# Performance work log

Hardware: AMD Instinct MI355X
Metric: run time of the kernel (lower is better)

## Reference

```python
import jax, jax.numpy as jnp
import numpy as np
import math

EMBED_DIM = 1024
NUM_HEADS = 16
HEAD_DIM = EMBED_DIM // NUM_HEADS
BLOCK_SIZE = 64
N_GLOBAL = 8


def _sparse_mask(seq_len: int) -> jnp.ndarray:
    """Block-diagonal local mask + 8 global tokens (rows and cols), bool [S, S]."""
    idx = jnp.arange(seq_len)
    block_id = idx // BLOCK_SIZE
    local = block_id[:, None] == block_id[None, :]
    # torch.linspace(0, S-1, min(8, S)).long() -> truncated evenly spaced positions
    gp = np.linspace(0, seq_len - 1, min(N_GLOBAL, seq_len)).astype(np.int64)
    is_global = jnp.zeros((seq_len,), dtype=bool).at[jnp.asarray(gp)].set(True)
    return local | is_global[:, None] | is_global[None, :]


def setup_inputs() -> dict:
    key = jax.random.key(0)
    ks = jax.random.split(key, 9)
    E = EMBED_DIM
    s = 0.02
    return {
        "x": jax.random.normal(ks[0], (1, 4096, E), dtype=jnp.float32),
        "Wq": jax.random.normal(ks[1], (E, E), dtype=jnp.float32) * s,
        "bq": jnp.zeros((E,), dtype=jnp.float32),
        "Wk": jax.random.normal(ks[2], (E, E), dtype=jnp.float32) * s,
        "bk": jnp.zeros((E,), dtype=jnp.float32),
        "Wv": jax.random.normal(ks[3], (E, E), dtype=jnp.float32) * s,
        "bv": jnp.zeros((E,), dtype=jnp.float32),
        "Wo": jax.random.normal(ks[4], (E, E), dtype=jnp.float32) * s,
        "bo": jnp.zeros((E,), dtype=jnp.float32),
    }


def reference(x, Wq, bq, Wk, bk, Wv, bv, Wo, bo):
    B, S, E = x.shape
    H, D = NUM_HEADS, HEAD_DIM
    mask = _sparse_mask(S)  # [S, S] bool

    def split_heads(y):
        return y.reshape(B, S, H, D).transpose(0, 2, 1, 3)  # [B,H,S,D]

    q = split_heads(x @ Wq + bq)
    k = split_heads(x @ Wk + bk)
    v = split_heads(x @ Wv + bv)

    scale = math.sqrt(D)
    scores = jnp.einsum("bhqd,bhkd->bhqk", q, k) / scale  # [B,H,S,S]
    scores = jnp.where(mask[None, None], scores, -jnp.inf)
    attn = jax.nn.softmax(scores, axis=-1)  # every row has its diagonal block -> no NaN
    out = jnp.einsum("bhqk,bhkd->bhqd", attn, v)
    out = out.transpose(0, 2, 1, 3).reshape(B, S, E)
    return out @ Wo + bo
```

## Files before the change

kernel.cpp:

```cpp
#include <hip/hip_runtime.h>

typedef __attribute__((ext_vector_type(8))) short short8;
typedef __attribute__((ext_vector_type(8))) __bf16 bf16x8;
typedef __attribute__((ext_vector_type(4))) float f32x4;

#define S_LEN 4096
#define EMB   1024
#define NHEAD 16
#define HDIM  64
#define GCHUNK 256
#define NCHUNK (S_LEN / GCHUNK)

__constant__ int GPOS[8] = {0, 585, 1170, 1755, 2340, 2925, 3510, 4095};

__device__ __forceinline__ unsigned short f2bf(float f) {
    unsigned int u = __float_as_uint(f);
    u += 0x7fffu + ((u >> 16) & 1u);
    return (unsigned short)(u >> 16);
}
__device__ __forceinline__ float bf2f(unsigned short s) {
    return __uint_as_float(((unsigned int)s) << 16);
}
#define GLOAD16(src, dst) __builtin_amdgcn_global_load_lds( \
    (const __attribute__((address_space(1))) void*)(src),    \
    (__attribute__((address_space(3))) void*)(dst), 16, 0, 0)

__global__ __launch_bounds__(256) void convert_x_kernel(const float4* __restrict__ in,
                                                        ushort4* __restrict__ out, int n4) {
    for (int i = blockIdx.x * blockDim.x + threadIdx.x; i < n4; i += gridDim.x * blockDim.x) {
        float4 v = in[i];
        ushort4 o;
        o.x = f2bf(v.x); o.y = f2bf(v.y); o.z = f2bf(v.z); o.w = f2bf(v.w);
        out[i] = o;
    }
}

__global__ __launch_bounds__(256) void convert_w_kernel(const float* __restrict__ W0,
                                                        const float* __restrict__ W1,
                                                        const float* __restrict__ W2,
                                                        const float* __restrict__ W3,
                                                        unsigned short* __restrict__ wt) {
    __shared__ float tile[64][65];
    const int bx = blockIdx.x;
    const int w = bx >> 8, rem = bx & 255;
    const int k0 = (rem >> 4) * 64, n0 = (rem & 15) * 64;
    const float* W = (w == 0) ? W0 : (w == 1) ? W1 : (w == 2) ? W2 : W3;
    unsigned short* dst = wt + (size_t)w * (1u << 20);
    const int t = threadIdx.x;
    for (int i = t; i < 4096; i += 256) {
        int r = i >> 6, c = i & 63;
        tile[r][c] = W[(size_t)(k0 + r) * EMB + n0 + c];
    }
    __syncthreads();
    for (int i = t; i < 4096; i += 256) {
        int r = i >> 6, c = i & 63;
        dst[(size_t)(n0 + r) * EMB + k0 + c] = f2bf(tile[c][r]);
    }
}

__global__ __launch_bounds__(256) void vtrans(const unsigned short* __restrict__ vb,
                                              unsigned short* __restrict__ vtg) {
    __shared__ unsigned short tile[64][72];
    const int t = threadIdx.x;
    const int h = blockIdx.x >> 6;
    const int s0 = (blockIdx.x & 63) * 64;
    for (int i = t; i < 512; i += 256) {
        int r = i >> 3, c = i & 7;
        *(short8*)&tile[r][c * 8] = *(const short8*)(vb + (size_t)(s0 + r) * EMB + h * 64 + c * 8);
    }
    __syncthreads();
    for (int i = t; i < 512; i += 256) {
        int d = i >> 3, c = i & 7;
        short8 v;
#pragma unroll
        for (int j = 0; j < 8; ++j) v[j] = (short)tile[c * 8 + j][d];
        *(short8*)(vtg + (size_t)(h * 64 + d) * S_LEN + s0 + c * 8) = v;
    }
}

__global__ __launch_bounds__(256) void gemm_qkv(const unsigned short* __restrict__ A,
                                                const unsigned short* __restrict__ Bt,
                                                const float* __restrict__ bq,
                                                const float* __restrict__ bk,
                                                const float* __restrict__ bv,
                                                unsigned short* __restrict__ qb,
                                                unsigned short* __restrict__ kb,
                                                unsigned short* __restrict__ vb) {
    __shared__ unsigned short As[128 * 64];
    __shared__ unsigned short Bs[128 * 64];
    const int t = threadIdx.x;
    const int lane = t & 63;
    const int wave = t >> 6;
    const int wm = wave >> 1, wn = wave & 1;
    const int col16 = lane & 15, grp = lane >> 4;
    const int bm = blockIdx.x / 24;
    const int bn = blockIdx.x % 24;
    const int sel = bn >> 3, bn_l = bn & 7;
    const float* bias = (sel == 0) ? bq : (sel == 1) ? bk : bv;
    unsigned short* out = (sel == 0) ? qb : (sel == 1) ? kb : vb;

    f32x4 acc[4][4] = {};

    for (int k0 = 0; k0 < EMB; k0 += 64) {
        __syncthreads();
#pragma unroll
        for (int c = 0; c < 8; ++c) {
            int p = t + 256 * (c & 3);
            int row = p >> 3, s = p & 7, kc = s ^ (row & 7);
            if (c < 4) {
                GLOAD16(A + (size_t)(bm * 128 + row) * EMB + k0 + kc * 8, As + p * 8);
            } else {
                GLOAD16(Bt + (size_t)(bn * 128 + row) * EMB + k0 + kc * 8, Bs + p * 8);
            }
        }
        asm volatile("s_waitcnt vmcnt(0)" ::: "memory");
        __syncthreads();
#pragma unroll
        for (int kk = 0; kk < 2; ++kk) {
            const int kc = kk * 4 + grp;
            bf16x8 af[4], bfr[4];
#pragma unroll
            for (int f = 0; f < 4; ++f) {
                int mrow = wm * 64 + f * 16 + col16;
                short8 ra = *(const short8*)(As + (mrow * 8 + (kc ^ (mrow & 7))) * 8);
                af[f] = __builtin_bit_cast(bf16x8, ra);
                int nrow = wn * 64 + f * 16 + col16;
                short8 rb = *(const short8*)(Bs + (nrow * 8 + (kc ^ (nrow & 7))) * 8);
                bfr[f] = __builtin_bit_cast(bf16x8, rb);
            }
#pragma unroll
            for (int fi = 0; fi < 4; ++fi)
#pragma unroll
                for (int fj = 0; fj < 4; ++fj)
                    acc[fi][fj] = __builtin_amdgcn_mfma_f32_16x16x32_bf16(af[fi], bfr[fj], acc[fi][fj], 0, 0, 0);
        }
    }

#pragma unroll
    for (int fi = 0; fi < 4; ++fi) {
        const int row0 = bm * 128 + wm * 64 + fi * 16 + grp * 4;
#pragma unroll
        for (int fj = 0; fj < 4; ++fj) {
            const int col = bn_l * 128 + wn * 64 + fj * 16 + col16;
            const float bvv = bias[col];
#pragma unroll
            for (int r = 0; r < 4; ++r)
                out[(size_t)(row0 + r) * EMB + col] = f2bf(acc[fi][fj][r] + bvv);
        }
    }
}

__global__ __launch_bounds__(256) void gemm_bt_f32(const unsigned short* __restrict__ A,
                                                   const unsigned short* __restrict__ Bt,
                                                   const float* __restrict__ bias,
                                                   float* __restrict__ Cout) {
    __shared__ unsigned short As[128 * 64];
    __shared__ unsigned short Bs[64 * 64];
    const int t = threadIdx.x;
    const int lane = t & 63;
    const int wave = t >> 6;
    const int wm = wave >> 1, wn = wave & 1;
    const int bm = blockIdx.x >> 4;
    const int bn = blockIdx.x & 15;

    f32x4 acc[4][2] = {};

    for (int k0 = 0; k0 < EMB; k0 += 64) {
        __syncthreads();
#pragma unroll
        for (int c = 0; c < 6; ++c) {
            const unsigned short* src;
            unsigned short* dst;
            if (c < 4) {
                int p = t + 256 * c;
                int m = p >> 3, s = p & 7;
                int kc = s ^ (m & 7);
                src = A + (size_t)(bm * 128 + m) * EMB + k0 + kc * 8;
                dst = As + p * 8;
            } else {
                int p = t + 256 * (c - 4);
                int n = p >> 3, s = p & 7;
                int kc = s ^ (n & 7);
                src = Bt + (size_t)(bn * 64 + n) * EMB + k0 + kc * 8;
                dst = Bs + p * 8;
            }
            GLOAD16(src, dst);
        }
        asm volatile("s_waitcnt vmcnt(0)" ::: "memory");
        __syncthreads();
#pragma unroll
        for (int kk = 0; kk < 2; ++kk) {
            const int kc = kk * 4 + (lane >> 4);
            bf16x8 af[4], bfr[2];
#pragma unroll
            for (int f = 0; f < 4; ++f) {
                int mrow = wm * 64 + f * 16 + (lane & 15);
                short8 ra = *(const short8*)(As + mrow * 64 + ((kc ^ (mrow & 7)) * 8));
                af[f] = __builtin_bit_cast(bf16x8, ra);
            }
#pragma unroll
            for (int f = 0; f < 2; ++f) {
                int nrow = wn * 32 + f * 16 + (lane & 15);
                short8 rb = *(const short8*)(Bs + nrow * 64 + ((kc ^ (nrow & 7)) * 8));
                bfr[f] = __builtin_bit_cast(bf16x8, rb);
            }
#pragma unroll
            for (int fi = 0; fi < 4; ++fi)
#pragma unroll
                for (int fj = 0; fj < 2; ++fj)
                    acc[fi][fj] = __builtin_amdgcn_mfma_f32_16x16x32_bf16(af[fi], bfr[fj], acc[fi][fj], 0, 0, 0);
        }
    }

#pragma unroll
    for (int fi = 0; fi < 4; ++fi) {
        const int row0 = bm * 128 + wm * 64 + fi * 16 + (lane >> 4) * 4;
#pragma unroll
        for (int fj = 0; fj < 2; ++fj) {
            const int col = bn * 64 + wn * 32 + fj * 16 + (lane & 15);
            const float bvv = bias[col];
#pragma unroll
            for (int r = 0; r < 4; ++r)
                Cout[(size_t)(row0 + r) * EMB + col] = acc[fi][fj][r] + bvv;
        }
    }
}

__global__ __launch_bounds__(256) void attn_local(const unsigned short* __restrict__ qb,
                                                  const unsigned short* __restrict__ kb,
                                                  const unsigned short* __restrict__ vb,
                                                  const unsigned short* __restrict__ vtg,
                                                  unsigned short* __restrict__ ab) {
    __shared__ unsigned short Qs[64 * 64];
    __shared__ unsigned short Ks[80 * 64];
    __shared__ unsigned short Vts[64 * 64];
    __shared__ unsigned short Ps[64 * 64];
    __shared__ float Pg[64][9];
    __shared__ float Vg[8][64];

    const int t = threadIdx.x;
    const int lane = t & 63, wave = t >> 6;
    const int col16 = lane & 15, grp = lane >> 4;
    const int h = blockIdx.x >> 6, b = blockIdx.x & 63;
    const int bc = h * 64;

#pragma unroll
    for (int c = 0; c < 2; ++c) {
        int p = t + 256 * c, row = p >> 3, s = p & 7, kc = s ^ (row & 7);
        GLOAD16(qb + (size_t)(b * 64 + row) * EMB + bc + kc * 8, Qs + p * 8);
    }
#pragma unroll
    for (int c = 0; c < 3; ++c) {
        int p = t + 256 * c;
        if (p < 576) {
            int row = p >> 3, s = p & 7, kc = s ^ (row & 7);
            int srow = (row < 64) ? (b * 64 + row) : GPOS[row - 64];
            GLOAD16(kb + (size_t)srow * EMB + bc + kc * 8, Ks + p * 8);
        }
    }
    if (t < 64) {
        short8 z = {};
        *(short8*)(Ks + (576 + t) * 8) = z;
    }
#pragma unroll
    for (int c = 0; c < 2; ++c) {
        int p = t + 256 * c, row = p >> 3, s = p & 7, kc = s ^ (row & 7);
        GLOAD16(vtg + (size_t)(bc + row) * S_LEN + b * 64 + kc * 8, Vts + p * 8);
    }
    for (int i = t; i < 512; i += 256) {
        int g = i >> 6, d = i & 63;
        Vg[g][d] = bf2f(vb[(size_t)GPOS[g] * EMB + bc + d]);
    }
    asm volatile("s_waitcnt vmcnt(0)" ::: "memory");
    __syncthreads();

    f32x4 sc[5] = {};
    const int arow = wave * 16 + col16;
#pragma unroll
    for (int kk = 0; kk < 2; ++kk) {
        const int kc = kk * 4 + (lane >> 4);
        short8 ra = *(const short8*)(Qs + (arow * 8 + (kc ^ (arow & 7))) * 8);
        bf16x8 af = __builtin_bit_cast(bf16x8, ra);
#pragma unroll
        for (int n = 0; n < 5; ++n) {
            const int brow = n * 16 + col16;
            short8 rb = *(const short8*)(Ks + (brow * 8 + (kc ^ (brow & 7))) * 8);
            sc[n] = __builtin_amdgcn_mfma_f32_16x16x32_bf16(af, __builtin_bit_cast(bf16x8, rb), sc[n], 0, 0, 0);
        }
    }

    const bool valid4 = (col16 < 8) && ((GPOS[col16] >> 6) != b);
#pragma unroll
    for (int r = 0; r < 4; ++r) {
        const int row = wave * 16 + grp * 4 + r;
        float s[5];
#pragma unroll
        for (int n = 0; n < 4; ++n) s[n] = sc[n][r] * 0.125f;
        s[4] = valid4 ? sc[4][r] * 0.125f : -1e30f;
        float m = fmaxf(fmaxf(fmaxf(s[0], s[1]), fmaxf(s[2], s[3])), s[4]);
#pragma unroll
        for (int off = 1; off < 16; off <<= 1) m = fmaxf(m, __shfl_xor(m, off));
        float e[5], l = 0.f;
#pragma unroll
        for (int n = 0; n < 5; ++n) { e[n] = __expf(s[n] - m); l += e[n]; }
#pragma unroll
        for (int off = 1; off < 16; off <<= 1) l += __shfl_xor(l, off);
        const float inv = 1.f / l;
#pragma unroll
        for (int n = 0; n < 4; ++n) {
            const int col = n * 16 + col16;
            const int kc = col >> 3;
            Ps[(row * 8 + (kc ^ (row & 7))) * 8 + (col & 7)] = f2bf(e[n] * inv);
        }
        if (col16 < 8) Pg[row][col16] = e[4] * inv;
    }
    __syncthreads();

    f32x4 oa[4] = {};
#pragma unroll
    for (int kk = 0; kk < 2; ++kk) {
        const int kc = kk * 4 + (lane >> 4);
        short8 ra = *(const short8*)(Ps + (arow * 8 + (kc ^ (arow & 7))) * 8);
        bf16x8 af = __builtin_bit_cast(bf16x8, ra);
#pragma unroll
        for (int n = 0; n < 4; ++n) {
            const int drow = n * 16 + col16;
            short8 rb = *(const short8*)(Vts + (drow * 8 + (kc ^ (drow & 7))) * 8);
            oa[n] = __builtin_amdgcn_mfma_f32_16x16x32_bf16(af, __builtin_bit_cast(bf16x8, rb), oa[n], 0, 0, 0);
        }
    }

    float pgr[4][8];
#pragma unroll
    for (int r = 0; r < 4; ++r) {
        const int row = wave * 16 + grp * 4 + r;
#pragma unroll
        for (int g = 0; g < 8; ++g) pgr[r][g] = Pg[row][g];
    }
#pragma unroll
    for (int n = 0; n < 4; ++n) {
        const int d = n * 16 + col16;
#pragma unroll
        for (int g = 0; g < 8; ++g) {
            const float vg = Vg[g][d];
#pragma unroll
            for (int r = 0; r < 4; ++r) oa[n][r] += pgr[r][g] * vg;
        }
    }

#pragma unroll
    for (int n = 0; n < 4; ++n) {
        const int d = n * 16 + col16;
#pragma unroll
        for (int r = 0; r < 4; ++r) {
            const int row = wave * 16 + grp * 4 + r;
            ab[(size_t)(b * 64 + row) * EMB + bc + d] = f2bf(oa[n][r]);
        }
    }
}

__global__ __launch_bounds__(256) void attn_gpart(const unsigned short* __restrict__ qb,
                                                  const unsigned short* __restrict__ kb,
                                                  const unsigned short* __restrict__ vb,
                                                  float* __restrict__ o_part,
                                                  float* __restrict__ m_l) {
    __shared__ float Qs[8][64];
    __shared__ unsigned short Vs[GCHUNK][64];
    __shared__ float Ps[8][GCHUNK];
    __shared__ float mfin[8], lfin[8];
    const int t = threadIdx.x;
    const int lane = t & 63;
    const int wave = t >> 6;
    const int h = blockIdx.x >> 4;
    const int ch = blockIdx.x & (NCHUNK - 1);
    const int bc = h * 64;
    const int k0 = ch * GCHUNK;

    for (int i = t; i < 512; i += 256) {
        int r = i >> 6, d = i & 63;
        Qs[r][d] = bf2f(qb[(size_t)GPOS[r] * EMB + bc + d]);
    }
    {
        const unsigned short* vrow = vb + (size_t)(k0 + t) * EMB + bc;
#pragma unroll
        for (int c = 0; c < 8; ++c) {
            short8 vv = *(const short8*)(vrow + c * 8);
            *(short8*)(&Vs[t][(c ^ (t & 7)) * 8]) = vv;
        }
    }
    float kf[64];
    {
        const unsigned short* krow = kb + (size_t)(k0 + t) * EMB + bc;
#pragma unroll
        for (int c = 0; c < 8; ++c) {
            short8 kv = *(const short8*)(krow + c * 8);
#pragma unroll
            for (int j = 0; j < 8; ++j) kf[c * 8 + j] = bf2f((unsigned short)kv[j]);
        }
    }
    __syncthreads();

#pragma unroll
    for (int r = 0; r < 8; ++r) {
        float a0 = 0.f, a1 = 0.f, a2 = 0.f, a3 = 0.f;
#pragma unroll
        for (int c4 = 0; c4 < 16; ++c4) {
            f32x4 q = *(const f32x4*)&Qs[r][c4 * 4];
            a0 += q.x * kf[c4 * 4 + 0];
            a1 += q.y * kf[c4 * 4 + 1];
            a2 += q.z * kf[c4 * 4 + 2];
            a3 += q.w * kf[c4 * 4 + 3];
        }
        Ps[r][t] = (a0 + a1 + a2 + a3) * 0.125f;
    }
    __syncthreads();

#pragma unroll
    for (int rr = 0; rr < 2; ++rr) {
        const int r = wave * 2 + rr;
        float v0 = Ps[r][lane], v1 = Ps[r][lane + 64], v2 = Ps[r][lane + 128], v3 = Ps[r][lane + 192];
        float m = fmaxf(fmaxf(v0, v1), fmaxf(v2, v3));
#pragma unroll
        for (int off = 1; off < 64; off <<= 1) m = fmaxf(m, __shfl_xor(m, off));
        float e0 = __expf(v0 - m), e1 = __expf(v1 - m), e2 = __expf(v2 - m), e3 = __expf(v3 - m);
        float l = e0 + e1 + e2 + e3;
#pragma unroll
        for (int off = 1; off < 64; off <<= 1) l += __shfl_xor(l, off);
        Ps[r][lane] = e0; Ps[r][lane + 64] = e1; Ps[r][lane + 128] = e2; Ps[r][lane + 192] = e3;
        if (lane == 0) { mfin[r] = m; lfin[r] = l; }
    }
    __syncthreads();

    const int r = t >> 5;
    const int d0 = (t & 31) * 2;
    const int cc = d0 >> 3, ee = d0 & 7;
    float acc0 = 0.f, acc1 = 0.f;
    for (int k = 0; k < GCHUNK; k += 4) {
        f32x4 p = *(const f32x4*)&Ps[r][k];
#pragma unroll
        for (int j = 0; j < 4; ++j) {
            unsigned int vv = *(const unsigned int*)&Vs[k + j][((cc ^ ((k + j) & 7)) << 3) + ee];
            acc0 += p[j] * bf2f((unsigned short)(vv & 0xffff));
            acc1 += p[j] * bf2f((unsigned short)(vv >> 16));
        }
    }
    const int rowg = h * 8 + r;
    float* od = o_part + ((size_t)rowg * NCHUNK + ch) * 64 + d0;
    od[0] = acc0; od[1] = acc1;
    if ((t & 31) == 0) {
        m_l[((size_t)rowg * NCHUNK + ch) * 2 + 0] = mfin[r];
        m_l[((size_t)rowg * NCHUNK + ch) * 2 + 1] = lfin[r];
    }
}

__global__ __launch_bounds__(256) void attn_gcomb(const float* __restrict__ o_part,
                                                  const float* __restrict__ m_l,
                                                  unsigned short* __restrict__ ab) {
    const int gid = blockIdx.x * 256 + threadIdx.x;
    const int row = gid >> 6, d = gid & 63;
    float M = -1e30f;
#pragma unroll
    for (int c = 0; c < NCHUNK; ++c) M = fmaxf(M, m_l[((size_t)row * NCHUNK + c) * 2]);
    float L = 0.f, o = 0.f;
#pragma unroll
    for (int c = 0; c < NCHUNK; ++c) {
        float w = __expf(m_l[((size_t)row * NCHUNK + c) * 2] - M);
        L += m_l[((size_t)row * NCHUNK + c) * 2 + 1] * w;
        o += o_part[((size_t)row * NCHUNK + c) * 64 + d] * w;
    }
    const int h = row >> 3, gi = row & 7;
    ab[(size_t)GPOS[gi] * EMB + h * 64 + d] = f2bf(o / L);
}

extern "C" void kernel_launch(void* const* d_in, const int* in_sizes, int n_in,
                              void* d_out, int out_size, void* d_ws, size_t ws_size,
                              hipStream_t stream) {
    const float* x  = (const float*)d_in[0];
    const float* Wq = (const float*)d_in[1];
    const float* bq = (const float*)d_in[2];
    const float* Wk = (const float*)d_in[3];
    const float* bk = (const float*)d_in[4];
    const float* Wv = (const float*)d_in[5];
    const float* bv = (const float*)d_in[6];
    const float* Wo = (const float*)d_in[7];
    const float* bo = (const float*)d_in[8];

    char* ws = (char*)d_ws;
    unsigned short* xb = (unsigned short*)ws;
    unsigned short* wt = (unsigned short*)(ws + (8u << 20));
    unsigned short* qb = (unsigned short*)(ws + (16u << 20));
    unsigned short* kb = (unsigned short*)(ws + (24u << 20));
    unsigned short* vb = (unsigned short*)(ws + (32u << 20));
    unsigned short* ab = xb;

    float* o_part = (float*)d_out;
    float* m_l    = (float*)d_out + 128 * NCHUNK * 64;
    unsigned short* vtg = (unsigned short*)((char*)d_out + (4u << 20));

    const int n4 = S_LEN * EMB / 4;
    convert_x_kernel<<<2048, 256, 0, stream>>>((const float4*)x, (ushort4*)xb, n4);
    convert_w_kernel<<<1024, 256, 0, stream>>>(Wq, Wk, Wv, Wo, wt);

    gemm_qkv<<<(S_LEN / 128) * 24, 256, 0, stream>>>(xb, wt, bq, bk, bv, qb, kb, vb);

    vtrans<<<1024, 256, 0, stream>>>(vb, vtg);
    attn_local<<<NHEAD * 64, 256, 0, stream>>>(qb, kb, vb, vtg, ab);
    attn_gpart<<<NHEAD * NCHUNK, 256, 0, stream>>>(qb, kb, vb, o_part, m_l);
    attn_gcomb<<<(128 * 64) / 256, 256, 0, stream>>>(o_part, m_l, ab);

    gemm_bt_f32<<<(S_LEN / 128) * 16, 256, 0, stream>>>(ab, wt + (3u << 20), bo, (float*)d_out);
}
```

Baseline: 109.5 us.

## Double-buffer LDS in QKV and output GEMMs and widen output tile

Both GEMM kernels now use two LDS buffers. The next K-slice is issued with global_load_lds while MFMAs run on the current slice, with a single barrier per iteration in place of the explicit vmcnt wait. The output projection GEMM also moves from 128x64 to 128x128 tiles, halving the grid to 256 blocks to improve operand reuse. The trade-offs are 64KB of LDS per block, which limits occupancy, and fewer blocks for the output GEMM. Correctness also relies on the barrier draining the outstanding LDS-DMA loads.

New measurement: 115.1 us. +5.2%, slower.

```diff
diff --git a/kernel.cpp b/kernel.cpp
--- a/kernel.cpp
+++ b/kernel.cpp
@@ -86,8 +86,8 @@
                                                 unsigned short* __restrict__ qb,
                                                 unsigned short* __restrict__ kb,
                                                 unsigned short* __restrict__ vb) {
-    __shared__ unsigned short As[128 * 64];
-    __shared__ unsigned short Bs[128 * 64];
+    __shared__ unsigned short As[2][128 * 64];
+    __shared__ unsigned short Bs[2][128 * 64];
     const int t = threadIdx.x;
     const int lane = t & 63;
     const int wave = t >> 6;
@@ -101,20 +101,31 @@
 
     f32x4 acc[4][4] = {};
 
-    for (int k0 = 0; k0 < EMB; k0 += 64) {
-        __syncthreads();
-#pragma unroll
-        for (int c = 0; c < 8; ++c) {
-            int p = t + 256 * (c & 3);
+    auto stage = [&](int buf, int tstep) {
+        const int k0 = tstep * 64;
+#pragma unroll
+        for (int c = 0; c < 4; ++c) {
+            int p = t + 256 * c;
             int row = p >> 3, s = p & 7, kc = s ^ (row & 7);
-            if (c < 4) {
-                GLOAD16(A + (size_t)(bm * 128 + row) * EMB + k0 + kc * 8, As + p * 8);
-            } else {
-                GLOAD16(Bt + (size_t)(bn * 128 + row) * EMB + k0 + kc * 8, Bs + p * 8);
-            }
-        }
-        asm volatile("s_waitcnt vmcnt(0)" ::: "memory");
-        __syncthreads();
+            GLOAD16(A + (size_t)(bm * 128 + row) * EMB + k0 + kc * 8, &As[buf][p * 8]);
+        }
+#pragma unroll
+        for (int c = 0; c < 4; ++c) {
+            int p = t + 256 * c;
+            int row = p >> 3, s = p & 7, kc = s ^ (row & 7);
+            GLOAD16(Bt + (size_t)(bn * 128 + row) * EMB + k0 + kc * 8, &Bs[buf][p * 8]);
+        }
+    };
+
+    stage(0, 0);
+    __syncthreads();
+
+#pragma unroll 2
+    for (int tstep = 0; tstep < 16; ++tstep) {
+        const int cur = tstep & 1;
+        if (tstep < 15) stage(cur ^ 1, tstep + 1);
+        const unsigned short* Ab = As[cur];
+        const unsigned short* Bb = Bs[cur];
 #pragma unroll
         for (int kk = 0; kk < 2; ++kk) {
             const int kc = kk * 4 + grp;
@@ -122,10 +133,10 @@
 #pragma unroll
             for (int f = 0; f < 4; ++f) {
                 int mrow = wm * 64 + f * 16 + col16;
-                short8 ra = *(const short8*)(As + (mrow * 8 + (kc ^ (mrow & 7))) * 8);
+                short8 ra = *(const short8*)(Ab + (mrow * 8 + (kc ^ (mrow & 7))) * 8);
                 af[f] = __builtin_bit_cast(bf16x8, ra);
                 int nrow = wn * 64 + f * 16 + col16;
-                short8 rb = *(const short8*)(Bs + (nrow * 8 + (kc ^ (nrow & 7))) * 8);
+                short8 rb = *(const short8*)(Bb + (nrow * 8 + (kc ^ (nrow & 7))) * 8);
                 bfr[f] = __builtin_bit_cast(bf16x8, rb);
             }
 #pragma unroll
@@ -134,6 +145,7 @@
                 for (int fj = 0; fj < 4; ++fj)
                     acc[fi][fj] = __builtin_amdgcn_mfma_f32_16x16x32_bf16(af[fi], bfr[fj], acc[fi][fj], 0, 0, 0);
         }
+        __syncthreads();
     }
 
 #pragma unroll
@@ -150,74 +162,75 @@
     }
 }
 
-__global__ __launch_bounds__(256) void gemm_bt_f32(const unsigned short* __restrict__ A,
-                                                   const unsigned short* __restrict__ Bt,
-                                                   const float* __restrict__ bias,
-                                                   float* __restrict__ Cout) {
-    __shared__ unsigned short As[128 * 64];
-    __shared__ unsigned short Bs[64 * 64];
+__global__ __launch_bounds__(256) void gemm_out(const unsigned short* __restrict__ A,
+                                                const unsigned short* __restrict__ Bt,
+                                                const float* __restrict__ bias,
+                                                float* __restrict__ Cout) {
+    __shared__ unsigned short As[2][128 * 64];
+    __shared__ unsigned short Bs[2][128 * 64];
     const int t = threadIdx.x;
     const int lane = t & 63;
     const int wave = t >> 6;
     const int wm = wave >> 1, wn = wave & 1;
-    const int bm = blockIdx.x >> 4;
-    const int bn = blockIdx.x & 15;
-
-    f32x4 acc[4][2] = {};
-
-    for (int k0 = 0; k0 < EMB; k0 += 64) {
-        __syncthreads();
-#pragma unroll
-        for (int c = 0; c < 6; ++c) {
-            const unsigned short* src;
-            unsigned short* dst;
-            if (c < 4) {
-                int p = t + 256 * c;
-                int m = p >> 3, s = p & 7;
-                int kc = s ^ (m & 7);
-                src = A + (size_t)(bm * 128 + m) * EMB + k0 + kc * 8;
-                dst = As + p * 8;
-            } else {
-                int p = t + 256 * (c - 4);
-                int n = p >> 3, s = p & 7;
-                int kc = s ^ (n & 7);
-                src = Bt + (size_t)(bn * 64 + n) * EMB + k0 + kc * 8;
-                dst = Bs + p * 8;
-            }
-            GLOAD16(src, dst);
-        }
-        asm volatile("s_waitcnt vmcnt(0)" ::: "memory");
-        __syncthreads();
+    const int col16 = lane & 15, grp = lane >> 4;
+    const int bm = blockIdx.x >> 3;
+    const int bn = blockIdx.x & 7;
+
+    f32x4 acc[4][4] = {};
+
+    auto stage = [&](int buf, int tstep) {
+        const int k0 = tstep * 64;
+#pragma unroll
+        for (int c = 0; c < 4; ++c) {
+            int p = t + 256 * c;
+            int row = p >> 3, s = p & 7, kc = s ^ (row & 7);
+            GLOAD16(A + (size_t)(bm * 128 + row) * EMB + k0 + kc * 8, &As[buf][p * 8]);
+        }
+#pragma unroll
+        for (int c = 0; c < 4; ++c) {
+            int p = t + 256 * c;
+            int row = p >> 3, s = p & 7, kc = s ^ (row & 7);
+            GLOAD16(Bt + (size_t)(bn * 128 + row) * EMB + k0 + kc * 8, &Bs[buf][p * 8]);
+        }
+    };
+
+    stage(0, 0);
+    __syncthreads();
+
+#pragma unroll 2
+    for (int tstep = 0; tstep < 16; ++tstep) {
+        const int cur = tstep & 1;
+        if (tstep < 15) stage(cur ^ 1, tstep + 1);
+        const unsigned short* Ab = As[cur];
+        const unsigned short* Bb = Bs[cur];
 #pragma unroll
         for (int kk = 0; kk < 2; ++kk) {
-            const int kc = kk * 4 + (lane >> 4);
-            bf16x8 af[4], bfr[2];
+            const int kc = kk * 4 + grp;
+            bf16x8 af[4], bfr[4];
 #pragma unroll
             for (int f = 0; f < 4; ++f) {
-                int mrow = wm * 64 + f * 16 + (lane & 15);
-                short8 ra = *(const short8*)(As + mrow * 64 + ((kc ^ (mrow & 7)) * 8));
+                int mrow = wm * 64 + f * 16 + col16;
+                short8 ra = *(const short8*)(Ab + (mrow * 8 + (kc ^ (mrow & 7))) * 8);
                 af[f] = __builtin_bit_cast(bf16x8, ra);
-            }
-#pragma unroll
-            for (int f = 0; f < 2; ++f) {
-                int nrow = wn * 32 + f * 16 + (lane & 15);
-                short8 rb = *(const short8*)(Bs + nrow * 64 + ((kc ^ (nrow & 7)) * 8));
+                int nrow = wn * 64 + f * 16 + col16;
+                short8 rb = *(const short8*)(Bb + (nrow * 8 + (kc ^ (nrow & 7))) * 8);
                 bfr[f] = __builtin_bit_cast(bf16x8, rb);
             }
 #pragma unroll
             for (int fi = 0; fi < 4; ++fi)
 #pragma unroll
-                for (int fj = 0; fj < 2; ++fj)
+                for (int fj = 0; fj < 4; ++fj)
                     acc[fi][fj] = __builtin_amdgcn_mfma_f32_16x16x32_bf16(af[fi], bfr[fj], acc[fi][fj], 0, 0, 0);
         }
+        __syncthreads();
     }
 
 #pragma unroll
     for (int fi = 0; fi < 4; ++fi) {
-        const int row0 = bm * 128 + wm * 64 + fi * 16 + (lane >> 4) * 4;
-#pragma unroll
-        for (int fj = 0; fj < 2; ++fj) {
-            const int col = bn * 64 + wn * 32 + fj * 16 + (lane & 15);
+        const int row0 = bm * 128 + wm * 64 + fi * 16 + grp * 4;
+#pragma unroll
+        for (int fj = 0; fj < 4; ++fj) {
+            const int col = bn * 128 + wn * 64 + fj * 16 + col16;
             const float bvv = bias[col];
 #pragma unroll
             for (int r = 0; r < 4; ++r)
@@ -508,5 +521,5 @@
     attn_gpart<<<NHEAD * NCHUNK, 256, 0, stream>>>(qb, kb, vb, o_part, m_l);
     attn_gcomb<<<(128 * 64) / 256, 256, 0, stream>>>(o_part, m_l, ab);
 
-    gemm_bt_f32<<<(S_LEN / 128) * 16, 256, 0, stream>>>(ab, wt + (3u << 20), bo, (float*)d_out);
-}
+    gemm_out<<<(S_LEN / 128) * 8, 256, 0, stream>>>(ab, wt + (3u << 20), bo, (float*)d_out);
+}
```
